# Optimization experiments

Hardware: AMD Instinct MI355X
Metric: run time of the kernel (lower is better)

The kernel has to match this reference:

```python
import jax, jax.numpy as jnp
import numpy as np

K = 3
KK = K * K
G = 8  # num_heads / offset groups
PAD = K // 2


def conv2d(x, w, b):
    # NCHW conv, stride 1, same padding
    y = jax.lax.conv_general_dilated(
        x, w, window_strides=(1, 1), padding=[(PAD, PAD), (PAD, PAD)],
        dimension_numbers=("NCHW", "OIHW", "NCHW"))
    return y + b[None, :, None, None]


def bilinear_sample(img, py, px):
    # img: [Cg, H, W]; py/px: [KK, H, W] fractional sampling locations
    # zero-padding bilinear (torchvision deform_conv2d semantics)
    Cg, H, W = img.shape
    flat = img.reshape(Cg, H * W)

    y0 = jnp.floor(py)
    x0 = jnp.floor(px)
    wy1 = py - y0
    wx1 = px - x0
    wy0 = 1.0 - wy1
    wx0 = 1.0 - wx1
    y0i = y0.astype(jnp.int32)
    x0i = x0.astype(jnp.int32)

    def gather(iy, ix):
        valid = (iy >= 0) & (iy < H) & (ix >= 0) & (ix < W)
        idx = jnp.clip(iy, 0, H - 1) * W + jnp.clip(ix, 0, W - 1)
        v = jnp.take(flat, idx.reshape(-1), axis=1).reshape(Cg, KK, H, W)
        return v * valid[None].astype(img.dtype)

    return (gather(y0i, x0i) * (wy0 * wx0)[None]
            + gather(y0i, x0i + 1) * (wy0 * wx1)[None]
            + gather(y0i + 1, x0i) * (wy1 * wx0)[None]
            + gather(y0i + 1, x0i + 1) * (wy1 * wx1)[None])


def setup_inputs() -> dict:
    key = jax.random.key(0)
    ks = jax.random.split(key, 8)
    B, C, H, W = 8, 256, 64, 64
    O = 256
    x = jax.random.normal(ks[0], (B, C, H, W), jnp.float32)
    w_off = jax.random.normal(ks[1], (2 * KK * G, C, K, K), jnp.float32) * 0.01
    b_off = jax.random.normal(ks[2], (2 * KK * G,), jnp.float32) * 0.01
    w_attn = jax.random.normal(ks[3], (KK * G, C, K, K), jnp.float32) * 0.01
    b_attn = jax.random.normal(ks[4], (KK * G,), jnp.float32) * 0.01
    w_out = jax.random.normal(ks[5], (O, C, K, K), jnp.float32) * 0.02
    b_out = jax.random.normal(ks[6], (O,), jnp.float32) * 0.01
    return {"x": x, "w_off": w_off, "b_off": b_off,
            "w_attn": w_attn, "b_attn": b_attn,
            "w_out": w_out, "b_out": b_out}


def reference(x, w_off, b_off, w_attn, b_attn, w_out, b_out):
    B, C, H, W = x.shape
    O = w_out.shape[0]
    Cg = C // G

    # learned offsets: [B, G, KK, 2(dy,dx), H, W]
    off = conv2d(x, w_off, b_off).reshape(B, G, KK, 2, H, W)
    # modulation mask with softmax over the KK kernel taps (per head)
    attn = conv2d(x, w_attn, b_attn).reshape(B, G, KK, H, W)
    attn = jax.nn.softmax(attn, axis=2)

    # base sampling grid for each kernel tap (stride=1, dilation=1)
    ki = (jnp.arange(KK) // K).astype(x.dtype)  # kernel row
    kj = (jnp.arange(KK) % K).astype(x.dtype)   # kernel col
    base_y = jnp.arange(H, dtype=x.dtype)[None, :, None] - PAD + ki[:, None, None]  # [KK,H,1]
    base_x = jnp.arange(W, dtype=x.dtype)[None, None, :] - PAD + kj[:, None, None]  # [KK,1,W]
    py = base_y + off[:, :, :, 0]  # [B,G,KK,H,W]
    px = base_x + off[:, :, :, 1]

    xg = x.reshape(B, G, Cg, H, W)
    # vmap bilinear gather over batch and offset groups -> [B,G,Cg,KK,H,W]
    samp = jax.vmap(jax.vmap(bilinear_sample))(xg, py, px)

    # modulated deformable conv: mask-weight the samples, contract with weights
    wt = w_out.reshape(O, G, Cg, KK)
    out = jnp.einsum("bgnkhw,bgkhw,ognk->bohw", samp, attn, wt)
    return out + b_out[None, :, None, None]
```

## Files before the change

kernel.cpp:

```cpp
#include <hip/hip_runtime.h>

#define BN   8
#define CC   256
#define HH   64
#define WW   64
#define GG   8
#define CG   32
#define KKK  9
#define OO   256
#define HW   (HH*WW)
#define NPAD 256
#define NOUT 216

#define XH   68
#define XROW (XH*256)
#define XB   (XH*XH*256)

typedef __attribute__((ext_vector_type(8))) _Float16 half8;
typedef __attribute__((ext_vector_type(4))) float f32x4;

union U4H8 { uint4 u; half8 h; };

#define LGKM0_BARRIER() do { \
    asm volatile("s_waitcnt lgkmcnt(0)" ::: "memory"); \
    __builtin_amdgcn_s_barrier(); \
    __builtin_amdgcn_sched_barrier(0); \
} while (0)

__global__ void repack_w(const float* __restrict__ w_out, _Float16* __restrict__ wt3) {
    int idx = blockIdx.x * 256 + threadIdx.x;
    if (idx >= GG * KKK * CG * OO) return;
    int e    = idx & 7;
    int lane = (idx >> 3) & 63;
    int ot   = (idx >> 9) & 15;
    int s    = idx >> 13;
    int kk = s % 9;
    int g  = s / 9;
    int oc = ot * 16 + (lane & 15);
    int cg = (lane >> 4) * 8 + e;
    wt3[idx] = (_Float16)w_out[oc * 2304 + (g * 32 + cg) * 9 + kk];
}

__global__ void repack_conv(const float* __restrict__ w_off, const float* __restrict__ b_off,
                            const float* __restrict__ w_attn, const float* __restrict__ b_attn,
                            _Float16* __restrict__ wt_conv, float* __restrict__ bias_c) {
    int idx = blockIdx.x * 256 + threadIdx.x;
    if (idx >= 9 * NPAD * 256) return;
    int e    = idx & 7;
    int lane = (idx >> 3) & 63;
    int ot   = (idx >> 9) & 15;
    int gs   = idx >> 13;
    int tap = gs >> 3;
    int ch  = (gs & 7) * 32 + (lane >> 4) * 8 + e;
    int n   = ot * 16 + (lane & 15);
    float v = 0.f;
    if (n < 144)      v = w_off[(n * 256 + ch) * 9 + tap];
    else if (n < 216) v = w_attn[((n - 144) * 256 + ch) * 9 + tap];
    wt_conv[idx] = (_Float16)v;
    if (idx < 224) {
        float bv = 0.f;
        if (idx < 144)      bv = b_off[idx];
        else if (idx < 216) bv = b_attn[idx - 144];
        bias_c[idx] = bv;
    }
}

__global__ __launch_bounds__(256) void repack_x(const float* __restrict__ x,
                                                _Float16* __restrict__ x_h) {
    __shared__ _Float16 T[64][264];
    const int bid = blockIdx.x;
    const int b = bid & 7, h = bid >> 3;
    const int t = threadIdx.x;
    const float* src = x + (((long)(b * 256 + t)) << 12) + h * 64;
    #pragma unroll
    for (int i = 0; i < 16; ++i) {
        float4 f = ((const float4*)src)[i];
        T[i * 4 + 0][t] = (_Float16)f.x;
        T[i * 4 + 1][t] = (_Float16)f.y;
        T[i * 4 + 2][t] = (_Float16)f.z;
        T[i * 4 + 3][t] = (_Float16)f.w;
    }
    __syncthreads();
    _Float16* dst = x_h + ((long)(b * XH + h + 2) * XH + 2) * 256;
    #pragma unroll
    for (int it = 0; it < 8; ++it) {
        int idx = it * 256 + t;
        int px = idx >> 5, ch = idx & 31;
        uint4 v = *(const uint4*)&T[px][ch * 8];
        *(uint4*)(dst + px * 256 + ch * 8) = v;
    }
}

__global__ __launch_bounds__(512, 4) void conv_mfma(
    const _Float16* __restrict__ x_h, const _Float16* __restrict__ wt_conv,
    const float* __restrict__ bias_c, float* __restrict__ conv_buf) {
    __shared__ alignas(16) char smem[36864];
    _Float16 (*Ald)[2][64][40] = (_Float16 (*)[2][64][40])smem;
    float* red = (float*)smem;

    const int bid = blockIdx.x;
    const int b = bid & 7, h = bid >> 3;
    const int t = threadIdx.x;
    const int lane = t & 63;
    const int wv = t >> 6;
    const int group = wv >> 2;
    const int wg = wv & 3;
    const int tl = t & 255;
    const int px = tl >> 2, cq = tl & 3;
    const int gs0 = group * 36;

    f32x4 acc[4][4];
    #pragma unroll
    for (int i = 0; i < 4; ++i)
        #pragma unroll
        for (int j = 0; j < 4; ++j) acc[i][j] = (f32x4){0.f, 0.f, 0.f, 0.f};

    const _Float16* xb = x_h + (long)b * XB + cq * 8;
    const _Float16* wB = wt_conv + (long)(wg * 256 + lane) * 8;

    uint4 aR;
    uint4 bq0, bq1, bq2, bq3;

    {
        int tap = gs0 >> 3, cc = gs0 & 7;
        int y = h + tap / 3 + 1, xc = px + tap % 3 + 1;
        uint4 a0 = *(const uint4*)(xb + ((long)(y * XH + xc)) * 256 + cc * 32);
        *(uint4*)&Ald[group][0][px][cq * 8] = a0;
    }
    {
        int gsn = gs0 + 1;
        int tap = gsn >> 3, cc = gsn & 7;
        int y = h + tap / 3 + 1, xc = px + tap % 3 + 1;
        aR = *(const uint4*)(xb + ((long)(y * XH + xc)) * 256 + cc * 32);
    }
    {
        const _Float16* wsB = wB + (long)gs0 * 8192;
        bq0 = *(const uint4*)(wsB);
        bq1 = *(const uint4*)(wsB + 512);
        bq2 = *(const uint4*)(wsB + 1024);
        bq3 = *(const uint4*)(wsB + 1536);
    }
    LGKM0_BARRIER();

    for (int s = 0; s < 36; ++s) {
        const int gs = gs0 + s;
        if (s < 35) {
            *(uint4*)&Ald[group][(s + 1) & 1][px][cq * 8] = aR;
        }
        if (s < 34) {
            int gsn = gs + 2;
            int tap = gsn >> 3, cc = gsn & 7;
            int y = h + tap / 3 + 1, xc = px + tap % 3 + 1;
            aR = *(const uint4*)(xb + ((long)(y * XH + xc)) * 256 + cc * 32);
        }
        {
            const int k0 = (lane >> 4) * 8;
            U4H8 b0, b1, b2, b3; b0.u = bq0; b1.u = bq1; b2.u = bq2; b3.u = bq3;
            #pragma unroll
            for (int mi = 0; mi < 4; ++mi) {
                half8 a = *(const half8*)&Ald[group][s & 1][mi * 16 + (lane & 15)][k0];
                acc[mi][0] = __builtin_amdgcn_mfma_f32_16x16x32_f16(a, b0.h, acc[mi][0], 0, 0, 0);
                acc[mi][1] = __builtin_amdgcn_mfma_f32_16x16x32_f16(a, b1.h, acc[mi][1], 0, 0, 0);
                acc[mi][2] = __builtin_amdgcn_mfma_f32_16x16x32_f16(a, b2.h, acc[mi][2], 0, 0, 0);
                acc[mi][3] = __builtin_amdgcn_mfma_f32_16x16x32_f16(a, b3.h, acc[mi][3], 0, 0, 0);
            }
        }
        if (s < 35) {
            const _Float16* wsB = wB + (long)(gs + 1) * 8192;
            bq0 = *(const uint4*)(wsB);
            bq1 = *(const uint4*)(wsB + 512);
            bq2 = *(const uint4*)(wsB + 1024);
            bq3 = *(const uint4*)(wsB + 1536);
        }
        LGKM0_BARRIER();
    }

    #pragma unroll
    for (int r = 0; r < 2; ++r) {
        __syncthreads();
        if (group == 1) {
            #pragma unroll
            for (int m2 = 0; m2 < 2; ++m2)
                #pragma unroll
                for (int j = 0; j < 4; ++j)
                    *(f32x4*)&red[tl * 36 + m2 * 16 + j * 4] = acc[r * 2 + m2][j];
        }
        __syncthreads();
        if (group == 0) {
            #pragma unroll
            for (int m2 = 0; m2 < 2; ++m2)
                #pragma unroll
                for (int j = 0; j < 4; ++j) {
                    f32x4 v = *(const f32x4*)&red[tl * 36 + m2 * 16 + j * 4];
                    acc[r * 2 + m2][j] += v;
                }
        }
    }

    if (group == 0) {
        const int colb = (lane >> 4) * 4;
        #pragma unroll
        for (int mi = 0; mi < 4; ++mi) {
            int px0 = mi * 16 + colb;
            #pragma unroll
            for (int j = 0; j < 4; ++j) {
                int oc = wg * 64 + j * 16 + (lane & 15);
                if (oc < NOUT) {
                    float bb = bias_c[oc];
                    float4 v = make_float4(acc[mi][j][0] + bb, acc[mi][j][1] + bb,
                                           acc[mi][j][2] + bb, acc[mi][j][3] + bb);
                    *(float4*)&conv_buf[((long)b * NOUT + oc) * HW + h * WW + px0] = v;
                }
            }
        }
    }
}

__device__ __forceinline__ void calc_coords(int h, int px, int ki, int kj,
    float dy, float dx, int& i00,
    float& u00, float& u01, float& u10, float& u11) {
    float py  = (float)(h - 1 + ki) + dy;
    float pxf = (float)(px - 1 + kj) + dx;
    float y0f = floorf(py), x0f = floorf(pxf);
    float wy1 = py - y0f, wx1 = pxf - x0f;
    float wy0 = 1.f - wy1, wx0 = 1.f - wx1;
    int y0 = min(max((int)y0f, -2), 64);
    int x0 = min(max((int)x0f, -2), 64);
    u00 = wy0 * wx0; u01 = wy0 * wx1;
    u10 = wy1 * wx0; u11 = wy1 * wx1;
    i00 = (y0 + 2) * XH + (x0 + 2);
}

__global__ __launch_bounds__(512, 4) void sample_gemm_mfma(
    const _Float16* __restrict__ x_h, const float* __restrict__ conv_buf,
    const _Float16* __restrict__ wt3,
    const float* __restrict__ b_out, float* __restrict__ out) {
    __shared__ alignas(16) char smem[38912];
    _Float16 (*Ald)[2][64][40] = (_Float16 (*)[2][64][40])smem;
    float* attnL = (float*)(smem + 20480);
    float* red = (float*)smem;

    const int bid = blockIdx.x;
    const int b = bid & 7, h = bid >> 3;
    const int t = threadIdx.x;
    const int lane = t & 63;
    const int wv = t >> 6;
    const int group = wv >> 2;
    const int wg = wv & 3;
    const int tl = t & 255;
    const int px = tl >> 2, cq = tl & 3;
    const int gs0 = group * 36;

    f32x4 acc[4][4];
    #pragma unroll
    for (int i = 0; i < 4; ++i)
        #pragma unroll
        for (int j = 0; j < 4; ++j) acc[i][j] = (f32x4){0.f, 0.f, 0.f, 0.f};

    const float* cbase = conv_buf + (long)b * NOUT * HW + h * WW;
    const _Float16* xbase = x_h + (long)b * XB + cq * 8;
    const _Float16* wB3 = wt3 + (long)(wg * 256 + lane) * 8;

    {
        int ppx = t & 63, g = t >> 6;
        const float* ap = cbase + (long)(144 + g * 9) * HW + ppx;
        float v[9];
        float m = -1e30f;
        #pragma unroll
        for (int k = 0; k < 9; ++k) { v[k] = ap[k * HW]; m = fmaxf(m, v[k]); }
        float ssum = 0.f;
        #pragma unroll
        for (int k = 0; k < 9; ++k) { v[k] = __expf(v[k] - m); ssum += v[k]; }
        float inv = 1.f / ssum;
        #pragma unroll
        for (int k = 0; k < 9; ++k) attnL[(g * 9 + k) * 64 + ppx] = v[k] * inv;
    }
    float dy0 = cbase[(2 * gs0) * HW + px], dx0 = cbase[(2 * gs0 + 1) * HW + px];
    __syncthreads();

    uint4 q00, q01, q10, q11;
    float u00, u01, u10, u11;
    float dyN, dxN;
    uint4 bq0, bq1, bq2, bq3;
    {
        int i00;
        float v00, v01, v10, v11;
        calc_coords(h, px, 0, 0, dy0, dx0, i00, v00, v01, v10, v11);
        const _Float16* xg = xbase + (group * 4) * 32 + (long)i00 * 256;
        uint4 a00 = *(const uint4*)(xg);
        uint4 a01 = *(const uint4*)(xg + 256);
        uint4 a10 = *(const uint4*)(xg + XROW);
        uint4 a11 = *(const uint4*)(xg + XROW + 256);
        float av = attnL[gs0 * 64 + px];
        U4H8 h00, h01, h10, h11;
        h00.u = a00; h01.u = a01; h10.u = a10; h11.u = a11;
        half8 rr = h00.h * (_Float16)v00 + h01.h * (_Float16)v01
                 + h10.h * (_Float16)v10 + h11.h * (_Float16)v11;
        rr = rr * (_Float16)av;
        *(half8*)&Ald[group][0][px][cq * 8] = rr;
    }
    {
        float dy1 = cbase[(2 * (gs0 + 1)) * HW + px];
        float dx1 = cbase[(2 * (gs0 + 1) + 1) * HW + px];
        int i00;
        calc_coords(h, px, 0, 1, dy1, dx1, i00, u00, u01, u10, u11);
        const _Float16* xg = xbase + (group * 4) * 32 + (long)i00 * 256;
        q00 = *(const uint4*)(xg);
        q01 = *(const uint4*)(xg + 256);
        q10 = *(const uint4*)(xg + XROW);
        q11 = *(const uint4*)(xg + XROW + 256);
        dyN = cbase[(2 * (gs0 + 2)) * HW + px];
        dxN = cbase[(2 * (gs0 + 2) + 1) * HW + px];
    }
    {
        const _Float16* wsB = wB3 + (long)gs0 * 8192;
        bq0 = *(const uint4*)(wsB);
        bq1 = *(const uint4*)(wsB + 512);
        bq2 = *(const uint4*)(wsB + 1024);
        bq3 = *(const uint4*)(wsB + 1536);
    }
    LGKM0_BARRIER();

    for (int s = 0; s < 36; ++s) {
        const int gs = gs0 + s;
        if (s < 35) {
            float av = attnL[(gs + 1) * 64 + px];
            U4H8 a00, a01, a10, a11;
            a00.u = q00; a01.u = q01; a10.u = q10; a11.u = q11;
            half8 rr = a00.h * (_Float16)u00 + a01.h * (_Float16)u01
                     + a10.h * (_Float16)u10 + a11.h * (_Float16)u11;
            rr = rr * (_Float16)av;
            *(half8*)&Ald[group][(s + 1) & 1][px][cq * 8] = rr;
        }
        if (s < 34) {
            int sn = s + 2;
            int g = group * 4 + sn / 9, kk = sn % 9;
            int i00;
            calc_coords(h, px, kk / 3, kk % 3, dyN, dxN, i00, u00, u01, u10, u11);
            const _Float16* xg = xbase + g * 32 + (long)i00 * 256;
            q00 = *(const uint4*)(xg);
            q01 = *(const uint4*)(xg + 256);
            q10 = *(const uint4*)(xg + XROW);
            q11 = *(const uint4*)(xg + XROW + 256);
            int s3 = min(s + 3, 35);
            dyN = cbase[(2 * (gs0 + s3)) * HW + px];
            dxN = cbase[(2 * (gs0 + s3) + 1) * HW + px];
        }
        {
            const int k0 = (lane >> 4) * 8;
            U4H8 b0, b1, b2, b3; b0.u = bq0; b1.u = bq1; b2.u = bq2; b3.u = bq3;
            #pragma unroll
            for (int mi = 0; mi < 4; ++mi) {
                half8 a = *(const half8*)&Ald[group][s & 1][mi * 16 + (lane & 15)][k0];
                acc[mi][0] = __builtin_amdgcn_mfma_f32_16x16x32_f16(a, b0.h, acc[mi][0], 0, 0, 0);
                acc[mi][1] = __builtin_amdgcn_mfma_f32_16x16x32_f16(a, b1.h, acc[mi][1], 0, 0, 0);
                acc[mi][2] = __builtin_amdgcn_mfma_f32_16x16x32_f16(a, b2.h, acc[mi][2], 0, 0, 0);
                acc[mi][3] = __builtin_amdgcn_mfma_f32_16x16x32_f16(a, b3.h, acc[mi][3], 0, 0, 0);
            }
        }
        if (s < 35) {
            const _Float16* wsB = wB3 + (long)(gs + 1) * 8192;
            bq0 = *(const uint4*)(wsB);
            bq1 = *(const uint4*)(wsB + 512);
            bq2 = *(const uint4*)(wsB + 1024);
            bq3 = *(const uint4*)(wsB + 1536);
        }
        LGKM0_BARRIER();
    }

    #pragma unroll
    for (int r = 0; r < 2; ++r) {
        __syncthreads();
        if (group == 1) {
            #pragma unroll
            for (int m2 = 0; m2 < 2; ++m2)
                #pragma unroll
                for (int j = 0; j < 4; ++j)
                    *(f32x4*)&red[tl * 36 + m2 * 16 + j * 4] = acc[r * 2 + m2][j];
        }
        __syncthreads();
        if (group == 0) {
            #pragma unroll
            for (int m2 = 0; m2 < 2; ++m2)
                #pragma unroll
                for (int j = 0; j < 4; ++j) {
                    f32x4 v = *(const f32x4*)&red[tl * 36 + m2 * 16 + j * 4];
                    acc[r * 2 + m2][j] += v;
                }
        }
    }

    if (group == 0) {
        const int colb = (lane >> 4) * 4;
        #pragma unroll
        for (int mi = 0; mi < 4; ++mi) {
            int px0 = mi * 16 + colb;
            #pragma unroll
            for (int j = 0; j < 4; ++j) {
                int oc = wg * 64 + j * 16 + (lane & 15);
                float bb = b_out[oc];
                float4 v = make_float4(acc[mi][j][0] + bb, acc[mi][j][1] + bb,
                                       acc[mi][j][2] + bb, acc[mi][j][3] + bb);
                *(float4*)&out[((long)b * OO + oc) * HW + h * WW + px0] = v;
            }
        }
    }
}

extern "C" void kernel_launch(void* const* d_in, const int* in_sizes, int n_in,
                              void* d_out, int out_size, void* d_ws, size_t ws_size,
                              hipStream_t stream) {
    const float* x      = (const float*)d_in[0];
    const float* w_off  = (const float*)d_in[1];
    const float* b_off  = (const float*)d_in[2];
    const float* w_attn = (const float*)d_in[3];
    const float* b_attn = (const float*)d_in[4];
    const float* w_out  = (const float*)d_in[5];
    const float* b_out  = (const float*)d_in[6];
    float* out = (float*)d_out;

    _Float16* x_h     = (_Float16*)d_ws;
    float* conv_buf   = (float*)(x_h + 9469952);
    _Float16* wt3     = (_Float16*)(conv_buf + 7077888);
    _Float16* wt_conv = wt3 + 589824;
    float* bias_c     = (float*)(wt_conv + 589824);

    hipMemsetAsync(x_h, 0, (size_t)9469952 * sizeof(_Float16), stream);

    repack_w<<<dim3((589824 + 255) / 256), dim3(256), 0, stream>>>(w_out, wt3);
    repack_conv<<<dim3((9 * NPAD * 256 + 255) / 256), dim3(256), 0, stream>>>(
        w_off, b_off, w_attn, b_attn, wt_conv, bias_c);
    repack_x<<<dim3(512), dim3(256), 0, stream>>>(x, x_h);

    conv_mfma<<<dim3(512), dim3(512), 0, stream>>>(x_h, wt_conv, bias_c, conv_buf);

    sample_gemm_mfma<<<dim3(512), dim3(512), 0, stream>>>(
        x_h, conv_buf, wt3, b_out, out);
}
```

Before: 215.9 us.

## Fuse offset conv with sampling GEMM and merge prep kernels into one

Merges the offset/attention convolution into the deformable sampling GEMM kernel, so the per-row conv results stay in LDS instead of making a round trip through a global conv_buf. The three repack kernels and the full-workspace memset are folded into one prep kernel that zeroes only the halo border of padded x_h. This removes about 28 MB of global traffic and several launches. In exchange, LDS per block rises to about 79 KB, which can lower occupancy below the requested 4 blocks per CU, and the two GEMM phases now run back to back inside each block.

```diff
diff --git a/kernel.cpp b/kernel.cpp
--- a/kernel.cpp
+++ b/kernel.cpp
@@ -16,6 +16,8 @@
 #define XROW (XH*256)
 #define XB   (XH*XH*256)
 
+#define COS  68
+
 typedef __attribute__((ext_vector_type(8))) _Float16 half8;
 typedef __attribute__((ext_vector_type(4))) float f32x4;
 
@@ -27,192 +29,85 @@
     __builtin_amdgcn_sched_barrier(0); \
 } while (0)
 
-__global__ void repack_w(const float* __restrict__ w_out, _Float16* __restrict__ wt3) {
-    int idx = blockIdx.x * 256 + threadIdx.x;
-    if (idx >= GG * KKK * CG * OO) return;
-    int e    = idx & 7;
-    int lane = (idx >> 3) & 63;
-    int ot   = (idx >> 9) & 15;
-    int s    = idx >> 13;
-    int kk = s % 9;
-    int g  = s / 9;
-    int oc = ot * 16 + (lane & 15);
-    int cg = (lane >> 4) * 8 + e;
-    wt3[idx] = (_Float16)w_out[oc * 2304 + (g * 32 + cg) * 9 + kk];
-}
-
-__global__ void repack_conv(const float* __restrict__ w_off, const float* __restrict__ b_off,
-                            const float* __restrict__ w_attn, const float* __restrict__ b_attn,
-                            _Float16* __restrict__ wt_conv, float* __restrict__ bias_c) {
-    int idx = blockIdx.x * 256 + threadIdx.x;
-    if (idx >= 9 * NPAD * 256) return;
-    int e    = idx & 7;
-    int lane = (idx >> 3) & 63;
-    int ot   = (idx >> 9) & 15;
-    int gs   = idx >> 13;
-    int tap = gs >> 3;
-    int ch  = (gs & 7) * 32 + (lane >> 4) * 8 + e;
-    int n   = ot * 16 + (lane & 15);
-    float v = 0.f;
-    if (n < 144)      v = w_off[(n * 256 + ch) * 9 + tap];
-    else if (n < 216) v = w_attn[((n - 144) * 256 + ch) * 9 + tap];
-    wt_conv[idx] = (_Float16)v;
-    if (idx < 224) {
-        float bv = 0.f;
-        if (idx < 144)      bv = b_off[idx];
-        else if (idx < 216) bv = b_attn[idx - 144];
-        bias_c[idx] = bv;
-    }
-}
-
-__global__ __launch_bounds__(256) void repack_x(const float* __restrict__ x,
-                                                _Float16* __restrict__ x_h) {
-    __shared__ _Float16 T[64][264];
+__global__ __launch_bounds__(256) void prep_all(
+    const float* __restrict__ x, const float* __restrict__ w_out,
+    const float* __restrict__ w_off, const float* __restrict__ b_off,
+    const float* __restrict__ w_attn, const float* __restrict__ b_attn,
+    _Float16* __restrict__ x_h, _Float16* __restrict__ wt3,
+    _Float16* __restrict__ wt_conv, float* __restrict__ bias_c) {
     const int bid = blockIdx.x;
-    const int b = bid & 7, h = bid >> 3;
     const int t = threadIdx.x;
-    const float* src = x + (((long)(b * 256 + t)) << 12) + h * 64;
-    #pragma unroll
-    for (int i = 0; i < 16; ++i) {
-        float4 f = ((const float4*)src)[i];
-        T[i * 4 + 0][t] = (_Float16)f.x;
-        T[i * 4 + 1][t] = (_Float16)f.y;
-        T[i * 4 + 2][t] = (_Float16)f.z;
-        T[i * 4 + 3][t] = (_Float16)f.w;
-    }
-    __syncthreads();
-    _Float16* dst = x_h + ((long)(b * XH + h + 2) * XH + 2) * 256;
-    #pragma unroll
-    for (int it = 0; it < 8; ++it) {
-        int idx = it * 256 + t;
-        int px = idx >> 5, ch = idx & 31;
-        uint4 v = *(const uint4*)&T[px][ch * 8];
-        *(uint4*)(dst + px * 256 + ch * 8) = v;
-    }
-}
-
-__global__ __launch_bounds__(512, 4) void conv_mfma(
-    const _Float16* __restrict__ x_h, const _Float16* __restrict__ wt_conv,
-    const float* __restrict__ bias_c, float* __restrict__ conv_buf) {
-    __shared__ alignas(16) char smem[36864];
-    _Float16 (*Ald)[2][64][40] = (_Float16 (*)[2][64][40])smem;
-    float* red = (float*)smem;
-
-    const int bid = blockIdx.x;
-    const int b = bid & 7, h = bid >> 3;
-    const int t = threadIdx.x;
-    const int lane = t & 63;
-    const int wv = t >> 6;
-    const int group = wv >> 2;
-    const int wg = wv & 3;
-    const int tl = t & 255;
-    const int px = tl >> 2, cq = tl & 3;
-    const int gs0 = group * 36;
-
-    f32x4 acc[4][4];
-    #pragma unroll
-    for (int i = 0; i < 4; ++i)
-        #pragma unroll
-        for (int j = 0; j < 4; ++j) acc[i][j] = (f32x4){0.f, 0.f, 0.f, 0.f};
-
-    const _Float16* xb = x_h + (long)b * XB + cq * 8;
-    const _Float16* wB = wt_conv + (long)(wg * 256 + lane) * 8;
-
-    uint4 aR;
-    uint4 bq0, bq1, bq2, bq3;
-
-    {
-        int tap = gs0 >> 3, cc = gs0 & 7;
-        int y = h + tap / 3 + 1, xc = px + tap % 3 + 1;
-        uint4 a0 = *(const uint4*)(xb + ((long)(y * XH + xc)) * 256 + cc * 32);
-        *(uint4*)&Ald[group][0][px][cq * 8] = a0;
-    }
-    {
-        int gsn = gs0 + 1;
-        int tap = gsn >> 3, cc = gsn & 7;
-        int y = h + tap / 3 + 1, xc = px + tap % 3 + 1;
-        aR = *(const uint4*)(xb + ((long)(y * XH + xc)) * 256 + cc * 32);
-    }
-    {
-        const _Float16* wsB = wB + (long)gs0 * 8192;
-        bq0 = *(const uint4*)(wsB);
-        bq1 = *(const uint4*)(wsB + 512);
-        bq2 = *(const uint4*)(wsB + 1024);
-        bq3 = *(const uint4*)(wsB + 1536);
-    }
-    LGKM0_BARRIER();
-
-    for (int s = 0; s < 36; ++s) {
-        const int gs = gs0 + s;
-        if (s < 35) {
-            *(uint4*)&Ald[group][(s + 1) & 1][px][cq * 8] = aR;
-        }
-        if (s < 34) {
-            int gsn = gs + 2;
-            int tap = gsn >> 3, cc = gsn & 7;
-            int y = h + tap / 3 + 1, xc = px + tap % 3 + 1;
-            aR = *(const uint4*)(xb + ((long)(y * XH + xc)) * 256 + cc * 32);
-        }
-        {
-            const int k0 = (lane >> 4) * 8;
-            U4H8 b0, b1, b2, b3; b0.u = bq0; b1.u = bq1; b2.u = bq2; b3.u = bq3;
-            #pragma unroll
-            for (int mi = 0; mi < 4; ++mi) {
-                half8 a = *(const half8*)&Ald[group][s & 1][mi * 16 + (lane & 15)][k0];
-                acc[mi][0] = __builtin_amdgcn_mfma_f32_16x16x32_f16(a, b0.h, acc[mi][0], 0, 0, 0);
-                acc[mi][1] = __builtin_amdgcn_mfma_f32_16x16x32_f16(a, b1.h, acc[mi][1], 0, 0, 0);
-                acc[mi][2] = __builtin_amdgcn_mfma_f32_16x16x32_f16(a, b2.h, acc[mi][2], 0, 0, 0);
-                acc[mi][3] = __builtin_amdgcn_mfma_f32_16x16x32_f16(a, b3.h, acc[mi][3], 0, 0, 0);
-            }
-        }
-        if (s < 35) {
-            const _Float16* wsB = wB + (long)(gs + 1) * 8192;
-            bq0 = *(const uint4*)(wsB);
-            bq1 = *(const uint4*)(wsB + 512);
-            bq2 = *(const uint4*)(wsB + 1024);
-            bq3 = *(const uint4*)(wsB + 1536);
-        }
-        LGKM0_BARRIER();
-    }
-
-    #pragma unroll
-    for (int r = 0; r < 2; ++r) {
+
+    if (bid < 512) {
+        __shared__ _Float16 T[64][264];
+        const int b = bid & 7, h = bid >> 3;
+        const float* src = x + (((long)(b * 256 + t)) << 12) + h * 64;
+        #pragma unroll
+        for (int i = 0; i < 16; ++i) {
+            float4 f = ((const float4*)src)[i];
+            T[i * 4 + 0][t] = (_Float16)f.x;
+            T[i * 4 + 1][t] = (_Float16)f.y;
+            T[i * 4 + 2][t] = (_Float16)f.z;
+            T[i * 4 + 3][t] = (_Float16)f.w;
+        }
         __syncthreads();
-        if (group == 1) {
-            #pragma unroll
-            for (int m2 = 0; m2 < 2; ++m2)
-                #pragma unroll
-                for (int j = 0; j < 4; ++j)
-                    *(f32x4*)&red[tl * 36 + m2 * 16 + j * 4] = acc[r * 2 + m2][j];
-        }
-        __syncthreads();
-        if (group == 0) {
-            #pragma unroll
-            for (int m2 = 0; m2 < 2; ++m2)
-                #pragma unroll
-                for (int j = 0; j < 4; ++j) {
-                    f32x4 v = *(const f32x4*)&red[tl * 36 + m2 * 16 + j * 4];
-                    acc[r * 2 + m2][j] += v;
-                }
-        }
-    }
-
-    if (group == 0) {
-        const int colb = (lane >> 4) * 4;
-        #pragma unroll
-        for (int mi = 0; mi < 4; ++mi) {
-            int px0 = mi * 16 + colb;
-            #pragma unroll
-            for (int j = 0; j < 4; ++j) {
-                int oc = wg * 64 + j * 16 + (lane & 15);
-                if (oc < NOUT) {
-                    float bb = bias_c[oc];
-                    float4 v = make_float4(acc[mi][j][0] + bb, acc[mi][j][1] + bb,
-                                           acc[mi][j][2] + bb, acc[mi][j][3] + bb);
-                    *(float4*)&conv_buf[((long)b * NOUT + oc) * HW + h * WW + px0] = v;
-                }
-            }
-        }
+        _Float16* dst = x_h + ((long)(b * XH + h + 2) * XH + 2) * 256;
+        #pragma unroll
+        for (int it = 0; it < 8; ++it) {
+            int idx = it * 256 + t;
+            int px = idx >> 5, ch = idx & 31;
+            uint4 v = *(const uint4*)&T[px][ch * 8];
+            *(uint4*)(dst + px * 256 + ch * 8) = v;
+        }
+    } else if (bid < 2816) {
+        int idx = (bid - 512) * 256 + t;
+        int e    = idx & 7;
+        int lane = (idx >> 3) & 63;
+        int ot   = (idx >> 9) & 15;
+        int s    = idx >> 13;
+        int kk = s % 9;
+        int g  = s / 9;
+        int oc = ot * 16 + (lane & 15);
+        int cg = (lane >> 4) * 8 + e;
+        wt3[idx] = (_Float16)w_out[oc * 2304 + (g * 32 + cg) * 9 + kk];
+    } else if (bid < 5120) {
+        int idx = (bid - 2816) * 256 + t;
+        int e    = idx & 7;
+        int lane = (idx >> 3) & 63;
+        int ot   = (idx >> 9) & 15;
+        int gs   = idx >> 13;
+        int tap = gs >> 3;
+        int ch  = (gs & 7) * 32 + (lane >> 4) * 8 + e;
+        int n   = ot * 16 + (lane & 15);
+        float v = 0.f;
+        if (n < 144)      v = w_off[(n * 256 + ch) * 9 + tap];
+        else if (n < 216) v = w_attn[((n - 144) * 256 + ch) * 9 + tap];
+        wt_conv[idx] = (_Float16)v;
+        if (idx < 224) {
+            float bv = 0.f;
+            if (idx < 144)      bv = b_off[idx];
+            else if (idx < 216) bv = b_attn[idx - 144];
+            bias_c[idx] = bv;
+        }
+    } else {
+        int gi = (bid - 5120) * 256 + t;
+        int b    = gi / 16896;
+        int r    = gi - b * 16896;
+        int cell = r >> 5;
+        int q    = r & 31;
+        int row, col;
+        if (cell < 272) {
+            int rr = cell / 68;
+            row = (rr < 2) ? rr : (rr + 64);
+            col = cell - rr * 68;
+        } else {
+            int cc = cell - 272;
+            row = 2 + (cc >> 2);
+            int ci = cc & 3;
+            col = (ci < 2) ? ci : (ci + 64);
+        }
+        _Float16* p = x_h + ((long)(b * XH + row) * XH + col) * 256 + q * 8;
+        *(uint4*)p = make_uint4(0u, 0u, 0u, 0u);
     }
 }
 
@@ -231,13 +126,13 @@
     i00 = (y0 + 2) * XH + (x0 + 2);
 }
 
-__global__ __launch_bounds__(512, 4) void sample_gemm_mfma(
-    const _Float16* __restrict__ x_h, const float* __restrict__ conv_buf,
-    const _Float16* __restrict__ wt3,
+__global__ __launch_bounds__(512, 4) void fused_mfma(
+    const _Float16* __restrict__ x_h, const _Float16* __restrict__ wt_conv,
+    const float* __restrict__ bias_c, const _Float16* __restrict__ wt3,
     const float* __restrict__ b_out, float* __restrict__ out) {
-    __shared__ alignas(16) char smem[38912];
-    _Float16 (*Ald)[2][64][40] = (_Float16 (*)[2][64][40])smem;
-    float* attnL = (float*)(smem + 20480);
+    __shared__ alignas(16) char smem[79232];
+    float* CO = (float*)smem;
+    _Float16 (*Ald)[2][64][40] = (_Float16 (*)[2][64][40])(smem + 58752);
     float* red = (float*)smem;
 
     const int bid = blockIdx.x;
@@ -250,158 +145,262 @@
     const int tl = t & 255;
     const int px = tl >> 2, cq = tl & 3;
     const int gs0 = group * 36;
-
-    f32x4 acc[4][4];
-    #pragma unroll
-    for (int i = 0; i < 4; ++i)
-        #pragma unroll
-        for (int j = 0; j < 4; ++j) acc[i][j] = (f32x4){0.f, 0.f, 0.f, 0.f};
-
-    const float* cbase = conv_buf + (long)b * NOUT * HW + h * WW;
-    const _Float16* xbase = x_h + (long)b * XB + cq * 8;
-    const _Float16* wB3 = wt3 + (long)(wg * 256 + lane) * 8;
+    const int colb = (lane >> 4) * 4;
+
+    const _Float16* xb = x_h + (long)b * XB + cq * 8;
+
+    {
+        f32x4 acc[4][4];
+        #pragma unroll
+        for (int i = 0; i < 4; ++i)
+            #pragma unroll
+            for (int j = 0; j < 4; ++j) acc[i][j] = (f32x4){0.f, 0.f, 0.f, 0.f};
+
+        const _Float16* wB = wt_conv + (long)(wg * 256 + lane) * 8;
+
+        uint4 aR;
+        uint4 bq0, bq1, bq2, bq3;
+
+        {
+            int gs = gs0;
+            int tap = gs >> 3, cc = gs & 7;
+            int y = h + tap / 3 + 1, xc = px + tap % 3 + 1;
+            uint4 a0 = *(const uint4*)(xb + ((long)(y * XH + xc)) * 256 + cc * 32);
+            *(uint4*)&Ald[group][0][px][cq * 8] = a0;
+        }
+        {
+            int gs = gs0 + 1;
+            int tap = gs >> 3, cc = gs & 7;
+            int y = h + tap / 3 + 1, xc = px + tap % 3 + 1;
+            aR = *(const uint4*)(xb + ((long)(y * XH + xc)) * 256 + cc * 32);
+        }
+        {
+            const _Float16* wsB = wB + (long)gs0 * 8192;
+            bq0 = *(const uint4*)(wsB);
+            bq1 = *(const uint4*)(wsB + 512);
+            bq2 = *(const uint4*)(wsB + 1024);
+            bq3 = *(const uint4*)(wsB + 1536);
+        }
+        LGKM0_BARRIER();
+
+        for (int s = 0; s < 36; ++s) {
+            if (s < 35) {
+                *(uint4*)&Ald[group][(s + 1) & 1][px][cq * 8] = aR;
+            }
+            if (s < 34) {
+                int gs = gs0 + s + 2;
+                int tap = gs >> 3, cc = gs & 7;
+                int y = h + tap / 3 + 1, xc = px + tap % 3 + 1;
+                aR = *(const uint4*)(xb + ((long)(y * XH + xc)) * 256 + cc * 32);
+            }
+            {
+                const int k0 = (lane >> 4) * 8;
+                U4H8 b0, b1, b2, b3; b0.u = bq0; b1.u = bq1; b2.u = bq2; b3.u = bq3;
+                #pragma unroll
+                for (int mi = 0; mi < 4; ++mi) {
+                    half8 a = *(const half8*)&Ald[group][s & 1][mi * 16 + (lane & 15)][k0];
+                    acc[mi][0] = __builtin_amdgcn_mfma_f32_16x16x32_f16(a, b0.h, acc[mi][0], 0, 0, 0);
+                    acc[mi][1] = __builtin_amdgcn_mfma_f32_16x16x32_f16(a, b1.h, acc[mi][1], 0, 0, 0);
+                    acc[mi][2] = __builtin_amdgcn_mfma_f32_16x16x32_f16(a, b2.h, acc[mi][2], 0, 0, 0);
+                    acc[mi][3] = __builtin_amdgcn_mfma_f32_16x16x32_f16(a, b3.h, acc[mi][3], 0, 0, 0);
+                }
+            }
+            if (s < 35) {
+                const _Float16* wsB = wB + (long)(gs0 + s + 1) * 8192;
+                bq0 = *(const uint4*)(wsB);
+                bq1 = *(const uint4*)(wsB + 512);
+                bq2 = *(const uint4*)(wsB + 1024);
+                bq3 = *(const uint4*)(wsB + 1536);
+            }
+            LGKM0_BARRIER();
+        }
+
+        if (group == 1) {
+            #pragma unroll
+            for (int mi = 0; mi < 4; ++mi) {
+                int px0 = mi * 16 + colb;
+                #pragma unroll
+                for (int j = 0; j < 4; ++j) {
+                    int oc = wg * 64 + j * 16 + (lane & 15);
+                    if (oc < NOUT) {
+                        float4 v = make_float4(acc[mi][j][0], acc[mi][j][1],
+                                               acc[mi][j][2], acc[mi][j][3]);
+                        *(float4*)&CO[oc * COS + px0] = v;
+                    }
+                }
+            }
+        }
+        __syncthreads();
+        if (group == 0) {
+            #pragma unroll
+            for (int mi = 0; mi < 4; ++mi) {
+                int px0 = mi * 16 + colb;
+                #pragma unroll
+                for (int j = 0; j < 4; ++j) {
+                    int oc = wg * 64 + j * 16 + (lane & 15);
+                    if (oc < NOUT) {
+                        float bb = bias_c[oc];
+                        float4 p = *(const float4*)&CO[oc * COS + px0];
+                        float4 v = make_float4(p.x + acc[mi][j][0] + bb,
+                                               p.y + acc[mi][j][1] + bb,
+                                               p.z + acc[mi][j][2] + bb,
+                                               p.w + acc[mi][j][3] + bb);
+                        *(float4*)&CO[oc * COS + px0] = v;
+                    }
+                }
+            }
+        }
+        __syncthreads();
+    }
 
     {
         int ppx = t & 63, g = t >> 6;
-        const float* ap = cbase + (long)(144 + g * 9) * HW + ppx;
+        float* ap = CO + (144 + g * 9) * COS + ppx;
         float v[9];
         float m = -1e30f;
         #pragma unroll
-        for (int k = 0; k < 9; ++k) { v[k] = ap[k * HW]; m = fmaxf(m, v[k]); }
+        for (int k = 0; k < 9; ++k) { v[k] = ap[k * COS]; m = fmaxf(m, v[k]); }
         float ssum = 0.f;
         #pragma unroll
         for (int k = 0; k < 9; ++k) { v[k] = __expf(v[k] - m); ssum += v[k]; }
         float inv = 1.f / ssum;
         #pragma unroll
-        for (int k = 0; k < 9; ++k) attnL[(g * 9 + k) * 64 + ppx] = v[k] * inv;
+        for (int k = 0; k < 9; ++k) ap[k * COS] = v[k] * inv;
     }
-    float dy0 = cbase[(2 * gs0) * HW + px], dx0 = cbase[(2 * gs0 + 1) * HW + px];
     __syncthreads();
 
-    uint4 q00, q01, q10, q11;
-    float u00, u01, u10, u11;
-    float dyN, dxN;
-    uint4 bq0, bq1, bq2, bq3;
     {
-        int i00;
-        float v00, v01, v10, v11;
-        calc_coords(h, px, 0, 0, dy0, dx0, i00, v00, v01, v10, v11);
-        const _Float16* xg = xbase + (group * 4) * 32 + (long)i00 * 256;
-        uint4 a00 = *(const uint4*)(xg);
-        uint4 a01 = *(const uint4*)(xg + 256);
-        uint4 a10 = *(const uint4*)(xg + XROW);
-        uint4 a11 = *(const uint4*)(xg + XROW + 256);
-        float av = attnL[gs0 * 64 + px];
-        U4H8 h00, h01, h10, h11;
-        h00.u = a00; h01.u = a01; h10.u = a10; h11.u = a11;
-        half8 rr = h00.h * (_Float16)v00 + h01.h * (_Float16)v01
-                 + h10.h * (_Float16)v10 + h11.h * (_Float16)v11;
-        rr = rr * (_Float16)av;
-        *(half8*)&Ald[group][0][px][cq * 8] = rr;
-    }
-    {
-        float dy1 = cbase[(2 * (gs0 + 1)) * HW + px];
-        float dx1 = cbase[(2 * (gs0 + 1) + 1) * HW + px];
-        int i00;
-        calc_coords(h, px, 0, 1, dy1, dx1, i00, u00, u01, u10, u11);
-        const _Float16* xg = xbase + (group * 4) * 32 + (long)i00 * 256;
-        q00 = *(const uint4*)(xg);
-        q01 = *(const uint4*)(xg + 256);
-        q10 = *(const uint4*)(xg + XROW);
-        q11 = *(const uint4*)(xg + XROW + 256);
-        dyN = cbase[(2 * (gs0 + 2)) * HW + px];
-        dxN = cbase[(2 * (gs0 + 2) + 1) * HW + px];
-    }
-    {
-        const _Float16* wsB = wB3 + (long)gs0 * 8192;
-        bq0 = *(const uint4*)(wsB);
-        bq1 = *(const uint4*)(wsB + 512);
-        bq2 = *(const uint4*)(wsB + 1024);
-        bq3 = *(const uint4*)(wsB + 1536);
-    }
-    LGKM0_BARRIER();
-
-    for (int s = 0; s < 36; ++s) {
-        const int gs = gs0 + s;
-        if (s < 35) {
-            float av = attnL[(gs + 1) * 64 + px];
-            U4H8 a00, a01, a10, a11;
-            a00.u = q00; a01.u = q01; a10.u = q10; a11.u = q11;
-            half8 rr = a00.h * (_Float16)u00 + a01.h * (_Float16)u01
-                     + a10.h * (_Float16)u10 + a11.h * (_Float16)u11;
+        f32x4 acc[4][4];
+        #pragma unroll
+        for (int i = 0; i < 4; ++i)
+            #pragma unroll
+            for (int j = 0; j < 4; ++j) acc[i][j] = (f32x4){0.f, 0.f, 0.f, 0.f};
+
+        const _Float16* xbase = xb;
+        const _Float16* wB3 = wt3 + (long)(wg * 256 + lane) * 8;
+
+        uint4 q00, q01, q10, q11;
+        float u00, u01, u10, u11;
+        uint4 bq0, bq1, bq2, bq3;
+
+        {
+            float dy0 = CO[(2 * gs0) * COS + px], dx0 = CO[(2 * gs0 + 1) * COS + px];
+            int i00;
+            float v00, v01, v10, v11;
+            calc_coords(h, px, 0, 0, dy0, dx0, i00, v00, v01, v10, v11);
+            const _Float16* xg = xbase + (group * 4) * 32 + (long)i00 * 256;
+            uint4 a00 = *(const uint4*)(xg);
+            uint4 a01 = *(const uint4*)(xg + 256);
+            uint4 a10 = *(const uint4*)(xg + XROW);
+            uint4 a11 = *(const uint4*)(xg + XROW + 256);
+            float av = CO[(144 + gs0) * COS + px];
+            U4H8 h00, h01, h10, h11;
+            h00.u = a00; h01.u = a01; h10.u = a10; h11.u = a11;
+            half8 rr = h00.h * (_Float16)v00 + h01.h * (_Float16)v01
+                     + h10.h * (_Float16)v10 + h11.h * (_Float16)v11;
             rr = rr * (_Float16)av;
-            *(half8*)&Ald[group][(s + 1) & 1][px][cq * 8] = rr;
-        }
-        if (s < 34) {
-            int sn = s + 2;
-            int g = group * 4 + sn / 9, kk = sn % 9;
+            *(half8*)&Ald[group][0][px][cq * 8] = rr;
+        }
+        {
+            float dy1 = CO[(2 * (gs0 + 1)) * COS + px];
+            float dx1 = CO[(2 * (gs0 + 1) + 1) * COS + px];
             int i00;
-            calc_coords(h, px, kk / 3, kk % 3, dyN, dxN, i00, u00, u01, u10, u11);
-            const _Float16* xg = xbase + g * 32 + (long)i00 * 256;
+            calc_coords(h, px, 0, 1, dy1, dx1, i00, u00, u01, u10, u11);
+            const _Float16* xg = xbase + (group * 4) * 32 + (long)i00 * 256;
             q00 = *(const uint4*)(xg);
             q01 = *(const uint4*)(xg + 256);
             q10 = *(const uint4*)(xg + XROW);
             q11 = *(const uint4*)(xg + XROW + 256);
-            int s3 = min(s + 3, 35);
-            dyN = cbase[(2 * (gs0 + s3)) * HW + px];
-            dxN = cbase[(2 * (gs0 + s3) + 1) * HW + px];
-        }
-        {
-            const int k0 = (lane >> 4) * 8;
-            U4H8 b0, b1, b2, b3; b0.u = bq0; b1.u = bq1; b2.u = bq2; b3.u = bq3;
-            #pragma unroll
-            for (int mi = 0; mi < 4; ++mi) {
-                half8 a = *(const half8*)&Ald[group][s & 1][mi * 16 + (lane & 15)][k0];
-                acc[mi][0] = __builtin_amdgcn_mfma_f32_16x16x32_f16(a, b0.h, acc[mi][0], 0, 0, 0);
-                acc[mi][1] = __builtin_amdgcn_mfma_f32_16x16x32_f16(a, b1.h, acc[mi][1], 0, 0, 0);
-                acc[mi][2] = __builtin_amdgcn_mfma_f32_16x16x32_f16(a, b2.h, acc[mi][2], 0, 0, 0);
-                acc[mi][3] = __builtin_amdgcn_mfma_f32_16x16x32_f16(a, b3.h, acc[mi][3], 0, 0, 0);
-            }
-        }
-        if (s < 35) {
-            const _Float16* wsB = wB3 + (long)(gs + 1) * 8192;
+        }
+        {
+            const _Float16* wsB = wB3 + (long)gs0 * 8192;
             bq0 = *(const uint4*)(wsB);
             bq1 = *(const uint4*)(wsB + 512);
             bq2 = *(const uint4*)(wsB + 1024);
             bq3 = *(const uint4*)(wsB + 1536);
         }
         LGKM0_BARRIER();
-    }
-
-    #pragma unroll
-    for (int r = 0; r < 2; ++r) {
-        __syncthreads();
-        if (group == 1) {
-            #pragma unroll
-            for (int m2 = 0; m2 < 2; ++m2)
-                #pragma unroll
-                for (int j = 0; j < 4; ++j)
-                    *(f32x4*)&red[tl * 36 + m2 * 16 + j * 4] = acc[r * 2 + m2][j];
-        }
-        __syncthreads();
+
+        for (int s = 0; s < 36; ++s) {
+            const int gs = gs0 + s;
+            if (s < 35) {
+                float av = CO[(144 + gs + 1) * COS + px];
+                U4H8 a00, a01, a10, a11;
+                a00.u = q00; a01.u = q01; a10.u = q10; a11.u = q11;
+                half8 rr = a00.h * (_Float16)u00 + a01.h * (_Float16)u01
+                         + a10.h * (_Float16)u10 + a11.h * (_Float16)u11;
+                rr = rr * (_Float16)av;
+                *(half8*)&Ald[group][(s + 1) & 1][px][cq * 8] = rr;
+            }
+            if (s < 34) {
+                int sn = s + 2;
+                int g = group * 4 + sn / 9, kk = sn % 9;
+                float dy = CO[(2 * (gs0 + sn)) * COS + px];
+                float dx = CO[(2 * (gs0 + sn) + 1) * COS + px];
+                int i00;
+                calc_coords(h, px, kk / 3, kk % 3, dy, dx, i00, u00, u01, u10, u11);
+                const _Float16* xg = xbase + g * 32 + (long)i00 * 256;
+                q00 = *(const uint4*)(xg);
+                q01 = *(const uint4*)(xg + 256);
+                q10 = *(const uint4*)(xg + XROW);
+                q11 = *(const uint4*)(xg + XROW + 256);
+            }
+            {
+                const int k0 = (lane >> 4) * 8;
+                U4H8 b0, b1, b2, b3; b0.u = bq0; b1.u = bq1; b2.u = bq2; b3.u = bq3;
+                #pragma unroll
+                for (int mi = 0; mi < 4; ++mi) {
+                    half8 a = *(const half8*)&Ald[group][s & 1][mi * 16 + (lane & 15)][k0];
+                    acc[mi][0] = __builtin_amdgcn_mfma_f32_16x16x32_f16(a, b0.h, acc[mi][0], 0, 0, 0);
+                    acc[mi][1] = __builtin_amdgcn_mfma_f32_16x16x32_f16(a, b1.h, acc[mi][1], 0, 0, 0);
+                    acc[mi][2] = __builtin_amdgcn_mfma_f32_16x16x32_f16(a, b2.h, acc[mi][2], 0, 0, 0);
+                    acc[mi][3] = __builtin_amdgcn_mfma_f32_16x16x32_f16(a, b3.h, acc[mi][3], 0, 0, 0);
+                }
+            }
+            if (s < 35) {
+                const _Float16* wsB = wB3 + (long)(gs + 1) * 8192;
+                bq0 = *(const uint4*)(wsB);
+                bq1 = *(const uint4*)(wsB + 512);
+                bq2 = *(const uint4*)(wsB + 1024);
+                bq3 = *(const uint4*)(wsB + 1536);
+            }
+            LGKM0_BARRIER();
+        }
+
+        #pragma unroll
+        for (int r = 0; r < 2; ++r) {
+            __syncthreads();
+            if (group == 1) {
+                #pragma unroll
+                for (int m2 = 0; m2 < 2; ++m2)
+                    #pragma unroll
+                    for (int j = 0; j < 4; ++j)
+                        *(f32x4*)&red[tl * 36 + m2 * 16 + j * 4] = acc[r * 2 + m2][j];
+            }
+            __syncthreads();
+            if (group == 0) {
+                #pragma unroll
+                for (int m2 = 0; m2 < 2; ++m2)
+                    #pragma unroll
+                    for (int j = 0; j < 4; ++j) {
+                        f32x4 v = *(const f32x4*)&red[tl * 36 + m2 * 16 + j * 4];
+                        acc[r * 2 + m2][j] += v;
+                    }
+            }
+        }
+
         if (group == 0) {
             #pragma unroll
-            for (int m2 = 0; m2 < 2; ++m2)
+            for (int mi = 0; mi < 4; ++mi) {
+                int px0 = mi * 16 + colb;
                 #pragma unroll
                 for (int j = 0; j < 4; ++j) {
-                    f32x4 v = *(const f32x4*)&red[tl * 36 + m2 * 16 + j * 4];
-                    acc[r * 2 + m2][j] += v;
+                    int oc = wg * 64 + j * 16 + (lane & 15);
+                    float bb = b_out[oc];
+                    float4 v = make_float4(acc[mi][j][0] + bb, acc[mi][j][1] + bb,
+                                           acc[mi][j][2] + bb, acc[mi][j][3] + bb);
+                    *(float4*)&out[((long)b * OO + oc) * HW + h * WW + px0] = v;
                 }
-        }
-    }
-
-    if (group == 0) {
-        const int colb = (lane >> 4) * 4;
-        #pragma unroll
-        for (int mi = 0; mi < 4; ++mi) {
-            int px0 = mi * 16 + colb;
-            #pragma unroll
-            for (int j = 0; j < 4; ++j) {
-                int oc = wg * 64 + j * 16 + (lane & 15);
-                float bb = b_out[oc];
-                float4 v = make_float4(acc[mi][j][0] + bb, acc[mi][j][1] + bb,
-                                       acc[mi][j][2] + bb, acc[mi][j][3] + bb);
-                *(float4*)&out[((long)b * OO + oc) * HW + h * WW + px0] = v;
             }
         }
     }
@@ -420,20 +419,13 @@
     float* out = (float*)d_out;
 
     _Float16* x_h     = (_Float16*)d_ws;
-    float* conv_buf   = (float*)(x_h + 9469952);
-    _Float16* wt3     = (_Float16*)(conv_buf + 7077888);
+    _Float16* wt3     = x_h + 9469952;
     _Float16* wt_conv = wt3 + 589824;
     float* bias_c     = (float*)(wt_conv + 589824);
 
-    hipMemsetAsync(x_h, 0, (size_t)9469952 * sizeof(_Float16), stream);
-
-    repack_w<<<dim3((589824 + 255) / 256), dim3(256), 0, stream>>>(w_out, wt3);
-    repack_conv<<<dim3((9 * NPAD * 256 + 255) / 256), dim3(256), 0, stream>>>(
-        w_off, b_off, w_attn, b_attn, wt_conv, bias_c);
-    repack_x<<<dim3(512), dim3(256), 0, stream>>>(x, x_h);
-
-    conv_mfma<<<dim3(512), dim3(512), 0, stream>>>(x_h, wt_conv, bias_c, conv_buf);
-
-    sample_gemm_mfma<<<dim3(512), dim3(512), 0, stream>>>(
-        x_h, conv_buf, wt3, b_out, out);
+    prep_all<<<dim3(5648), dim3(256), 0, stream>>>(
+        x, w_out, w_off, b_off, w_attn, b_attn, x_h, wt3, wt_conv, bias_c);
+
+    fused_mfma<<<dim3(512), dim3(512), 0, stream>>>(
+        x_h, wt_conv, bias_c, wt3, b_out, out);
 }
```

Measured after the change: 207.0 us. 1.04x faster.
